# Kernel optimization log

Hardware: AMD Instinct MI355X
Metric: run time of the kernel (lower is better)

The kernel has to match this reference:

```python
import jax, jax.numpy as jnp
import numpy as np

B, T, I, E, K, J = 4, 4096, 1024, 16, 512, 1024


def setup_inputs() -> dict:
    key = jax.random.key(0)
    k1, k2, k3 = jax.random.split(key, 3)
    X = jax.random.normal(k1, (B, T, I), dtype=jnp.float32)
    ind = jax.random.randint(k2, (B, E, K), 0, T, dtype=jnp.int64)
    bound = 1.0 / np.sqrt(J)
    W = jax.random.uniform(k3, (E, I, J), dtype=jnp.float32, minval=-bound, maxval=bound)
    return {"X": X, "ind": ind, "W": W}


def reference(X, ind, W):
    Bs, Ts, Is = X.shape
    _, Es, Ks = ind.shape
    # gather tokens per expert: [B, E*K, I] -> [B, E, K, I]
    idx = ind.reshape(Bs, Es * Ks)
    Xg = jnp.take_along_axis(X, idx[:, :, None], axis=1).reshape(Bs, Es, Ks, Is)
    # per-expert GEMM
    Y = jnp.einsum('beki,eij->bekj', Xg, W)
    return Y
```

## Files before the change

kernel.cpp:

```cpp
#include <hip/hip_runtime.h>
#include <cstdint>
#include <cstddef>


typedef float    floatx4 __attribute__((ext_vector_type(4)));
typedef _Float16 half8   __attribute__((ext_vector_type(8)));

constexpr int Bc = 4, Tc = 4096, Ic = 1024, Ec = 16, Kc = 512, Jc = 1024;
constexpr int BM = 256, BN = 256, BK = 64, NT = 512;
constexpr int NKT = Ic / BK;
constexpr int UNIT = 16384;
constexpr int BOFF = 4 * UNIT;

__device__ __forceinline__ void async16(const void* g, void* l) {
  __builtin_amdgcn_global_load_lds(
      (const __attribute__((address_space(1))) uint32_t*)g,
      (__attribute__((address_space(3))) uint32_t*)l, 16, 0, 0);
}

__global__ void cvt_kernel(const float* __restrict__ X, _Float16* __restrict__ Xh, int n8,
                           const float* __restrict__ W, _Float16* __restrict__ WT) {
  __shared__ float tile[64][65];
  const int bidx = blockIdx.x;
  if (bidx >= Ec * 256) {
    int i = (bidx - Ec * 256) * blockDim.x + threadIdx.x;
    const int stride = 2048 * blockDim.x;
    for (; i < n8; i += stride) {
      floatx4 v0 = ((const floatx4*)X)[2 * i];
      floatx4 v1 = ((const floatx4*)X)[2 * i + 1];
      half8 h;
      h[0] = (_Float16)v0.x; h[1] = (_Float16)v0.y; h[2] = (_Float16)v0.z; h[3] = (_Float16)v0.w;
      h[4] = (_Float16)v1.x; h[5] = (_Float16)v1.y; h[6] = (_Float16)v1.z; h[7] = (_Float16)v1.w;
      ((half8*)Xh)[i] = h;
    }
    return;
  }
  const int bid = bidx;
  const int e  = bid >> 8;
  const int i0 = ((bid >> 4) & 15) * 64;
  const int j0 = (bid & 15) * 64;
  const int tid = threadIdx.x;
  const int r  = tid >> 4;
  const int c4 = tid & 15;
  const float* src = W + ((size_t)e << 20) + (size_t)i0 * Jc + j0;
#pragma unroll
  for (int s = 0; s < 4; s++) {
    int rr = r + s * 16;
    floatx4 v = *(const floatx4*)(src + (size_t)rr * Jc + c4 * 4);
    tile[rr][c4 * 4 + 0] = v.x; tile[rr][c4 * 4 + 1] = v.y;
    tile[rr][c4 * 4 + 2] = v.z; tile[rr][c4 * 4 + 3] = v.w;
  }
  __syncthreads();
  const int jj = tid >> 2;
  const int ig = tid & 3;
  half8 hv0, hv1;
#pragma unroll
  for (int q = 0; q < 8; q++) hv0[q] = (_Float16)tile[ig * 16 + q][jj];
#pragma unroll
  for (int q = 0; q < 8; q++) hv1[q] = (_Float16)tile[ig * 16 + 8 + q][jj];
  _Float16* dst = WT + ((size_t)e << 20) + (size_t)(j0 + jj) * Ic + i0 + ig * 16;
  ((half8*)dst)[0] = hv0;
  ((half8*)dst)[1] = hv1;
}

__global__ __launch_bounds__(NT, 2) void gemm_kernel(
    const int* __restrict__ ind32,
    const _Float16* __restrict__ Xh, const _Float16* __restrict__ WT,
    float* __restrict__ Y) {
  __shared__ alignas(16) unsigned char smem[8 * UNIT];
  __shared__ int rowid[BM];
  __shared__ int is64_s;
  float* lbuf = (float*)smem;
  char* smemc = (char*)smem;

  const int tid = threadIdx.x;
  const int bid = blockIdx.x;
  const int x = bid & 7, s = (bid >> 3) & 7, chunk = bid >> 6;
  const int g = chunk * 8 + x;
  const int e = g >> 2, nt = g & 3;
  const int b = s >> 1, mt = s & 1;
  const int be = b * Ec + e;
  const int k0 = mt * BM;
  const int j0 = nt * BN;

  if (tid < 64) {
    int v = ind32[2 * tid + 1];
    unsigned long long m = __ballot(v != 0);
    if (tid == 0) is64_s = (m == 0ULL) ? 1 : 0;
  }
  __syncthreads();
  if (tid < BM) {
    int idx = be * Kc + k0 + tid;
    rowid[tid] = is64_s ? ind32[2 * idx] : ind32[idx];
  }
  __syncthreads();

  const int lane = tid & 63;
  const int wave = tid >> 6;
  const int wmb = (wave >> 2) * 128;
  const int wnb = (wave & 3) * 64;
  const int quad = lane >> 4;
  const int tr = lane & 15;

  const _Float16* aSrc[2];
  const _Float16* bSrc[2];
#pragma unroll
  for (int q = 0; q < 2; q++) {
    const int sl = wave * 128 + q * 64 + lane;
    const int r2 = sl >> 3, p = sl & 7;
    const int pos = p ^ (r2 & 7);
    const int r = 2 * r2 + (pos >> 2);
    const int c = pos & 3;
    aSrc[q] = Xh + ((size_t)b * Tc + rowid[r]) * Ic + c * 8;
    bSrc[q] = WT + ((size_t)e * Jc + j0 + r) * Ic + c * 8;
  }
  const int wdst = wave * 2048;

  int offA[2][4], offB[4];
#pragma unroll
  for (int mh = 0; mh < 2; mh++)
#pragma unroll
    for (int mi = 0; mi < 4; mi++) {
      const int R = wmb + mh * 64 + mi * 16 + tr;
      const int r2 = R >> 1;
      offA[mh][mi] = r2 * 128 + ((((R & 1) << 2) | quad) ^ (r2 & 7)) * 16;
    }
#pragma unroll
  for (int ni = 0; ni < 4; ni++) {
    const int R = wnb + ni * 16 + tr;
    const int r2 = R >> 1;
    offB[ni] = r2 * 128 + ((((R & 1) << 2) | quad) ^ (r2 & 7)) * 16;
  }

  floatx4 acc[8][4];
#pragma unroll
  for (int mi = 0; mi < 8; mi++)
#pragma unroll
    for (int ni = 0; ni < 4; ni++) acc[mi][ni] = {0.f, 0.f, 0.f, 0.f};

#define STAGE_A(TT, KS) do { \
    char* d_ = smemc + ((2 * (TT) + (KS)) & 3) * UNIT + wdst; \
    async16(aSrc[0] + (TT) * 64 + (KS) * 32, d_); \
    async16(aSrc[1] + (TT) * 64 + (KS) * 32, d_ + 1024); \
  } while (0)
#define STAGE_B(TT, KS) do { \
    char* d_ = smemc + BOFF + ((2 * (TT) + (KS)) & 3) * UNIT + wdst; \
    async16(bSrc[0] + (TT) * 64 + (KS) * 32, d_); \
    async16(bSrc[1] + (TT) * 64 + (KS) * 32, d_ + 1024); \
  } while (0)

#define PHASE(SK, MH, STAGE_STMT, CLOSE_STMT) do { \
    const char* Ab_ = smemc + (SK) * UNIT; \
    const char* Bb_ = smemc + BOFF + (SK) * UNIT; \
    half8 af_[4], bf_[4]; \
    _Pragma("unroll") \
    for (int mi_ = 0; mi_ < 4; mi_++) af_[mi_] = *(const half8*)(Ab_ + offA[MH][mi_]); \
    _Pragma("unroll") \
    for (int ni_ = 0; ni_ < 4; ni_++) bf_[ni_] = *(const half8*)(Bb_ + offB[ni_]); \
    STAGE_STMT \
    __builtin_amdgcn_s_barrier(); \
    asm volatile("s_waitcnt lgkmcnt(0)" ::: "memory"); \
    __builtin_amdgcn_sched_barrier(0); \
    __builtin_amdgcn_s_setprio(1); \
    _Pragma("unroll") \
    for (int mi_ = 0; mi_ < 4; mi_++) \
      _Pragma("unroll") \
      for (int ni_ = 0; ni_ < 4; ni_++) \
        acc[(MH) * 4 + mi_][ni_] = __builtin_amdgcn_mfma_f32_16x16x32_f16( \
            af_[mi_], bf_[ni_], acc[(MH) * 4 + mi_][ni_], 0, 0, 0); \
    __builtin_amdgcn_s_setprio(0); \
    CLOSE_STMT \
    __builtin_amdgcn_s_barrier(); \
  } while (0)

  STAGE_A(0, 0); STAGE_B(0, 0);
  STAGE_A(0, 1); STAGE_B(0, 1);
  STAGE_A(1, 0); STAGE_B(1, 0);
  asm volatile("s_waitcnt vmcnt(4)" ::: "memory");
  __builtin_amdgcn_s_barrier();

#pragma unroll 2
  for (int t = 0; t < NKT; t++) {
    const int sk0 = (2 * t) & 3;
    const int sk1 = sk0 + 1;
    const bool f1 = (t + 1 < NKT);
    const bool f2 = (t + 2 < NKT);
    PHASE(sk0, 0, { if (f1) STAGE_A(t + 1, 1); }, {});
    PHASE(sk0, 1, { if (f1) STAGE_B(t + 1, 1); }, {});
    PHASE(sk1, 0, { if (f2) STAGE_A(t + 2, 0); }, {});
    PHASE(sk1, 1, { if (f2) STAGE_B(t + 2, 0); },
          { if (t == NKT - 2) { asm volatile("s_waitcnt vmcnt(0)" ::: "memory"); }
            else if (t < NKT - 2) { asm volatile("s_waitcnt vmcnt(4)" ::: "memory"); } });
  }
#undef PHASE
#undef STAGE_A
#undef STAGE_B

  constexpr int LST = 257;
  float* Yb = Y + (size_t)be * Kc * Jc;
#pragma unroll
  for (int pass = 0; pass < 8; pass++) {
    if ((wave >> 2) == (pass >> 2)) {
#pragma unroll
      for (int h = 0; h < 2; h++) {
        const int mi = (pass & 3) * 2 + h;
        const int rr = h * 16 + quad * 4;
#pragma unroll
        for (int ni = 0; ni < 4; ni++) {
          const int col = wnb + ni * 16 + tr;
#pragma unroll
          for (int r = 0; r < 4; r++)
            lbuf[(rr + r) * LST + col] = acc[mi][ni][r];
        }
      }
    }
    __syncthreads();
#pragma unroll
    for (int it = 0; it < 4; it++) {
      const int idx = tid + it * NT;
      const int rr = idx >> 6, c4 = idx & 63;
      floatx4 v = *(const floatx4*)&lbuf[rr * LST + c4 * 4];
      *(floatx4*)&Yb[(size_t)(k0 + pass * 32 + rr) * Jc + j0 + c4 * 4] = v;
    }
    __syncthreads();
  }
}

extern "C" void kernel_launch(void* const* d_in, const int* in_sizes, int n_in,
                              void* d_out, int out_size, void* d_ws, size_t ws_size,
                              hipStream_t stream) {
  const float* X = (const float*)d_in[0];
  const int* ind = (const int*)d_in[1];
  const float* W = (const float*)d_in[2];
  float* Y = (float*)d_out;

  const size_t nx = (size_t)Bc * Tc * Ic;
  _Float16* Xh = (_Float16*)d_ws;
  _Float16* WT = Xh + nx;

  cvt_kernel<<<Ec * 256 + 2048, 256, 0, stream>>>(X, Xh, (int)(nx / 8), W, WT);
  const int gemm_grid = (Bc * Ec) * (Kc / BM) * (Jc / BN);
  gemm_kernel<<<gemm_grid, NT, 0, stream>>>(ind, Xh, WT, Y);
}
```

Measured before the change: 314.4 us.

## Restructure GEMM main loop to share B fragments and cut barriers per k-tile

Replaces the four barrier-separated phases per k-tile with two half-steps. Each half-step loads the B fragments once and reuses them across both M halves, and stage issues are interleaved with the LDS fragment loads. The last two iterations are peeled so the steady-state loop has no prefetch conditionals. This cuts LDS traffic and the number of barriers per iteration, but drops the explicit lgkmcnt waits and sched_barrier. Instruction ordering is left to the compiler, and register pressure rises from holding three fragment arrays.

```diff
diff --git a/kernel.cpp b/kernel.cpp
--- a/kernel.cpp
+++ b/kernel.cpp
@@ -149,28 +149,25 @@
     async16(bSrc[1] + (TT) * 64 + (KS) * 32, d_ + 1024); \
   } while (0)
 
-#define PHASE(SK, MH, STAGE_STMT, CLOSE_STMT) do { \
+#define LDAF(DST, SK, MH) do { \
     const char* Ab_ = smemc + (SK) * UNIT; \
+    _Pragma("unroll") \
+    for (int mi_ = 0; mi_ < 4; mi_++) DST[mi_] = *(const half8*)(Ab_ + offA[MH][mi_]); \
+  } while (0)
+#define LDBF(DST, SK) do { \
     const char* Bb_ = smemc + BOFF + (SK) * UNIT; \
-    half8 af_[4], bf_[4]; \
     _Pragma("unroll") \
-    for (int mi_ = 0; mi_ < 4; mi_++) af_[mi_] = *(const half8*)(Ab_ + offA[MH][mi_]); \
-    _Pragma("unroll") \
-    for (int ni_ = 0; ni_ < 4; ni_++) bf_[ni_] = *(const half8*)(Bb_ + offB[ni_]); \
-    STAGE_STMT \
-    __builtin_amdgcn_s_barrier(); \
-    asm volatile("s_waitcnt lgkmcnt(0)" ::: "memory"); \
-    __builtin_amdgcn_sched_barrier(0); \
+    for (int ni_ = 0; ni_ < 4; ni_++) DST[ni_] = *(const half8*)(Bb_ + offB[ni_]); \
+  } while (0)
+#define MFMA16(MH, AF, BF) do { \
     __builtin_amdgcn_s_setprio(1); \
     _Pragma("unroll") \
     for (int mi_ = 0; mi_ < 4; mi_++) \
       _Pragma("unroll") \
       for (int ni_ = 0; ni_ < 4; ni_++) \
         acc[(MH) * 4 + mi_][ni_] = __builtin_amdgcn_mfma_f32_16x16x32_f16( \
-            af_[mi_], bf_[ni_], acc[(MH) * 4 + mi_][ni_], 0, 0, 0); \
+            AF[mi_], BF[ni_], acc[(MH) * 4 + mi_][ni_], 0, 0, 0); \
     __builtin_amdgcn_s_setprio(0); \
-    CLOSE_STMT \
-    __builtin_amdgcn_s_barrier(); \
   } while (0)
 
   STAGE_A(0, 0); STAGE_B(0, 0);
@@ -179,22 +176,68 @@
   asm volatile("s_waitcnt vmcnt(4)" ::: "memory");
   __builtin_amdgcn_s_barrier();
 
-#pragma unroll 2
-  for (int t = 0; t < NKT; t++) {
-    const int sk0 = (2 * t) & 3;
-    const int sk1 = sk0 + 1;
-    const bool f1 = (t + 1 < NKT);
-    const bool f2 = (t + 2 < NKT);
-    PHASE(sk0, 0, { if (f1) STAGE_A(t + 1, 1); }, {});
-    PHASE(sk0, 1, { if (f1) STAGE_B(t + 1, 1); }, {});
-    PHASE(sk1, 0, { if (f2) STAGE_A(t + 2, 0); }, {});
-    PHASE(sk1, 1, { if (f2) STAGE_B(t + 2, 0); },
-          { if (t == NKT - 2) { asm volatile("s_waitcnt vmcnt(0)" ::: "memory"); }
-            else if (t < NKT - 2) { asm volatile("s_waitcnt vmcnt(4)" ::: "memory"); } });
-  }
-#undef PHASE
+  for (int t = 0; t < NKT - 2; ++t) {
+    const int sk0 = (2 * t) & 3, sk1 = sk0 + 1;
+    half8 af0[4], af1[4], bf[4];
+    LDAF(af0, sk0, 0);
+    LDBF(bf, sk0);
+    STAGE_A(t + 1, 1);
+    LDAF(af1, sk0, 1);
+    STAGE_B(t + 1, 1);
+    MFMA16(0, af0, bf);
+    MFMA16(1, af1, bf);
+    __builtin_amdgcn_s_barrier();
+    LDAF(af1, sk1, 1);
+    LDBF(bf, sk1);
+    STAGE_A(t + 2, 0);
+    LDAF(af0, sk1, 0);
+    STAGE_B(t + 2, 0);
+    MFMA16(1, af1, bf);
+    MFMA16(0, af0, bf);
+    asm volatile("s_waitcnt vmcnt(4)" ::: "memory");
+    __builtin_amdgcn_s_barrier();
+  }
+  {
+    const int t = NKT - 2;
+    const int sk0 = (2 * t) & 3, sk1 = sk0 + 1;
+    half8 af0[4], af1[4], bf[4];
+    LDAF(af0, sk0, 0);
+    LDBF(bf, sk0);
+    STAGE_A(t + 1, 1);
+    LDAF(af1, sk0, 1);
+    STAGE_B(t + 1, 1);
+    MFMA16(0, af0, bf);
+    MFMA16(1, af1, bf);
+    __builtin_amdgcn_s_barrier();
+    LDAF(af1, sk1, 1);
+    LDBF(bf, sk1);
+    LDAF(af0, sk1, 0);
+    MFMA16(1, af1, bf);
+    MFMA16(0, af0, bf);
+    asm volatile("s_waitcnt vmcnt(0)" ::: "memory");
+    __builtin_amdgcn_s_barrier();
+  }
+  {
+    const int t = NKT - 1;
+    const int sk0 = (2 * t) & 3, sk1 = sk0 + 1;
+    half8 af0[4], af1[4], bf[4];
+    LDAF(af0, sk0, 0);
+    LDBF(bf, sk0);
+    LDAF(af1, sk0, 1);
+    MFMA16(0, af0, bf);
+    MFMA16(1, af1, bf);
+    LDAF(af1, sk1, 1);
+    LDBF(bf, sk1);
+    LDAF(af0, sk1, 0);
+    MFMA16(1, af1, bf);
+    MFMA16(0, af0, bf);
+  }
+  __syncthreads();
+#undef MFMA16
+#undef LDBF
+#undef LDAF
+#undef STAGE_B
 #undef STAGE_A
-#undef STAGE_B
 
   constexpr int LST = 257;
   float* Yb = Y + (size_t)be * Kc * Jc;
```

New measurement: 309.9 us. About the same (-1.4%).

## Shrink LDS ring to 80KB with 3-slot A, 2-slot B pipeline for higher occupancy

Applied to the files above, without the earlier changes.

Restructures the software pipeline so each phase consumes a full 32-wide k-step across all 8 M sub-tiles. A uses a 3-slot ring and B a 2-slot ring, with the loop unrolled by 6 to keep slot indices static. Shared memory drops from 128KB to 80KB and the row-id scratch is folded into the ring. Launch bounds are raised to 4 waves per SIMD so more blocks can be resident and memory latency is hidden better. The costs are more register pressure from holding 8 A fragments under the tighter register budget, and a shallower B prefetch distance.

```diff
diff --git a/kernel.cpp b/kernel.cpp
--- a/kernel.cpp
+++ b/kernel.cpp
@@ -7,10 +7,10 @@
 typedef _Float16 half8   __attribute__((ext_vector_type(8)));
 
 constexpr int Bc = 4, Tc = 4096, Ic = 1024, Ec = 16, Kc = 512, Jc = 1024;
-constexpr int BM = 256, BN = 256, BK = 64, NT = 512;
-constexpr int NKT = Ic / BK;
+constexpr int BM = 256, BN = 256, NT = 512;
 constexpr int UNIT = 16384;
-constexpr int BOFF = 4 * UNIT;
+constexpr int A_RING = 3 * UNIT;
+constexpr int SMEM_BYTES = A_RING + 2 * UNIT;
 
 __device__ __forceinline__ void async16(const void* g, void* l) {
   __builtin_amdgcn_global_load_lds(
@@ -63,15 +63,14 @@
   ((half8*)dst)[1] = hv1;
 }
 
-__global__ __launch_bounds__(NT, 2) void gemm_kernel(
+__global__ __launch_bounds__(NT, 4) void gemm_kernel(
     const int* __restrict__ ind32,
     const _Float16* __restrict__ Xh, const _Float16* __restrict__ WT,
     float* __restrict__ Y) {
-  __shared__ alignas(16) unsigned char smem[8 * UNIT];
-  __shared__ int rowid[BM];
-  __shared__ int is64_s;
+  __shared__ alignas(16) unsigned char smem[SMEM_BYTES];
+  char* smemc = (char*)smem;
+  int* itmp = (int*)smem;
   float* lbuf = (float*)smem;
-  char* smemc = (char*)smem;
 
   const int tid = threadIdx.x;
   const int bid = blockIdx.x;
@@ -86,12 +85,13 @@
   if (tid < 64) {
     int v = ind32[2 * tid + 1];
     unsigned long long m = __ballot(v != 0);
-    if (tid == 0) is64_s = (m == 0ULL) ? 1 : 0;
-  }
-  __syncthreads();
+    if (tid == 0) itmp[256] = (m == 0ULL) ? 1 : 0;
+  }
+  __syncthreads();
+  const int is64 = itmp[256];
   if (tid < BM) {
     int idx = be * Kc + k0 + tid;
-    rowid[tid] = is64_s ? ind32[2 * idx] : ind32[idx];
+    itmp[tid] = is64 ? ind32[2 * idx] : ind32[idx];
   }
   __syncthreads();
 
@@ -111,20 +111,19 @@
     const int pos = p ^ (r2 & 7);
     const int r = 2 * r2 + (pos >> 2);
     const int c = pos & 3;
-    aSrc[q] = Xh + ((size_t)b * Tc + rowid[r]) * Ic + c * 8;
+    aSrc[q] = Xh + ((size_t)b * Tc + itmp[r]) * Ic + c * 8;
     bSrc[q] = WT + ((size_t)e * Jc + j0 + r) * Ic + c * 8;
   }
   const int wdst = wave * 2048;
-
-  int offA[2][4], offB[4];
-#pragma unroll
-  for (int mh = 0; mh < 2; mh++)
-#pragma unroll
-    for (int mi = 0; mi < 4; mi++) {
-      const int R = wmb + mh * 64 + mi * 16 + tr;
-      const int r2 = R >> 1;
-      offA[mh][mi] = r2 * 128 + ((((R & 1) << 2) | quad) ^ (r2 & 7)) * 16;
-    }
+  __syncthreads();
+
+  int offA[8], offB[4];
+#pragma unroll
+  for (int mi = 0; mi < 8; mi++) {
+    const int R = wmb + mi * 16 + tr;
+    const int r2 = R >> 1;
+    offA[mi] = r2 * 128 + ((((R & 1) << 2) | quad) ^ (r2 & 7)) * 16;
+  }
 #pragma unroll
   for (int ni = 0; ni < 4; ni++) {
     const int R = wnb + ni * 16 + tr;
@@ -138,63 +137,62 @@
 #pragma unroll
     for (int ni = 0; ni < 4; ni++) acc[mi][ni] = {0.f, 0.f, 0.f, 0.f};
 
-#define STAGE_A(TT, KS) do { \
-    char* d_ = smemc + ((2 * (TT) + (KS)) & 3) * UNIT + wdst; \
-    async16(aSrc[0] + (TT) * 64 + (KS) * 32, d_); \
-    async16(aSrc[1] + (TT) * 64 + (KS) * 32, d_ + 1024); \
+#define STAGE_A(U, SL) do { \
+    char* d_ = smemc + (SL) * UNIT + wdst; \
+    async16(aSrc[0] + (U) * 32, d_); \
+    async16(aSrc[1] + (U) * 32, d_ + 1024); \
   } while (0)
-#define STAGE_B(TT, KS) do { \
-    char* d_ = smemc + BOFF + ((2 * (TT) + (KS)) & 3) * UNIT + wdst; \
-    async16(bSrc[0] + (TT) * 64 + (KS) * 32, d_); \
-    async16(bSrc[1] + (TT) * 64 + (KS) * 32, d_ + 1024); \
+#define STAGE_B(U, SL) do { \
+    char* d_ = smemc + A_RING + (SL) * UNIT + wdst; \
+    async16(bSrc[0] + (U) * 32, d_); \
+    async16(bSrc[1] + (U) * 32, d_ + 1024); \
   } while (0)
 
-#define PHASE(SK, MH, STAGE_STMT, CLOSE_STMT) do { \
-    const char* Ab_ = smemc + (SK) * UNIT; \
-    const char* Bb_ = smemc + BOFF + (SK) * UNIT; \
-    half8 af_[4], bf_[4]; \
+#define PHASE(ASL, BSL, DOB, DOA, CLOSE) do { \
+    const char* Ab_ = smemc + (ASL) * UNIT; \
+    const char* Bb_ = smemc + A_RING + (BSL) * UNIT; \
+    half8 af_[8], bf_[4]; \
     _Pragma("unroll") \
-    for (int mi_ = 0; mi_ < 4; mi_++) af_[mi_] = *(const half8*)(Ab_ + offA[MH][mi_]); \
+    for (int mi_ = 0; mi_ < 8; mi_++) af_[mi_] = *(const half8*)(Ab_ + offA[mi_]); \
     _Pragma("unroll") \
     for (int ni_ = 0; ni_ < 4; ni_++) bf_[ni_] = *(const half8*)(Bb_ + offB[ni_]); \
-    STAGE_STMT \
+    DOB; DOA; \
     __builtin_amdgcn_s_barrier(); \
     asm volatile("s_waitcnt lgkmcnt(0)" ::: "memory"); \
     __builtin_amdgcn_sched_barrier(0); \
     __builtin_amdgcn_s_setprio(1); \
     _Pragma("unroll") \
-    for (int mi_ = 0; mi_ < 4; mi_++) \
+    for (int mi_ = 0; mi_ < 8; mi_++) \
       _Pragma("unroll") \
       for (int ni_ = 0; ni_ < 4; ni_++) \
-        acc[(MH) * 4 + mi_][ni_] = __builtin_amdgcn_mfma_f32_16x16x32_f16( \
-            af_[mi_], bf_[ni_], acc[(MH) * 4 + mi_][ni_], 0, 0, 0); \
+        acc[mi_][ni_] = __builtin_amdgcn_mfma_f32_16x16x32_f16( \
+            af_[mi_], bf_[ni_], acc[mi_][ni_], 0, 0, 0); \
     __builtin_amdgcn_s_setprio(0); \
-    CLOSE_STMT \
+    CLOSE; \
     __builtin_amdgcn_s_barrier(); \
   } while (0)
 
-  STAGE_A(0, 0); STAGE_B(0, 0);
-  STAGE_A(0, 1); STAGE_B(0, 1);
-  STAGE_A(1, 0); STAGE_B(1, 0);
-  asm volatile("s_waitcnt vmcnt(4)" ::: "memory");
+  STAGE_A(0, 0); STAGE_B(0, 0); STAGE_A(1, 1);
+  asm volatile("s_waitcnt vmcnt(2)" ::: "memory");
   __builtin_amdgcn_s_barrier();
 
-#pragma unroll 2
-  for (int t = 0; t < NKT; t++) {
-    const int sk0 = (2 * t) & 3;
-    const int sk1 = sk0 + 1;
-    const bool f1 = (t + 1 < NKT);
-    const bool f2 = (t + 2 < NKT);
-    PHASE(sk0, 0, { if (f1) STAGE_A(t + 1, 1); }, {});
-    PHASE(sk0, 1, { if (f1) STAGE_B(t + 1, 1); }, {});
-    PHASE(sk1, 0, { if (f2) STAGE_A(t + 2, 0); }, {});
-    PHASE(sk1, 1, { if (f2) STAGE_B(t + 2, 0); },
-          { if (t == NKT - 2) { asm volatile("s_waitcnt vmcnt(0)" ::: "memory"); }
-            else if (t < NKT - 2) { asm volatile("s_waitcnt vmcnt(4)" ::: "memory"); } });
-  }
+  for (int u0 = 0; u0 < 30; u0 += 6) {
+#pragma unroll
+    for (int i = 0; i < 6; i++) {
+      const int u = u0 + i;
+      PHASE(i % 3, i & 1,
+            STAGE_B(u + 1, (i + 1) & 1),
+            STAGE_A(u + 2, (i + 2) % 3),
+            asm volatile("s_waitcnt vmcnt(2)" ::: "memory"));
+    }
+  }
+  PHASE(0, 0, STAGE_B(31, 1), (void)0,
+        asm volatile("s_waitcnt vmcnt(0)" ::: "memory"));
+  PHASE(1, 1, (void)0, (void)0, (void)0);
+  __syncthreads();
 #undef PHASE
+#undef STAGE_B
 #undef STAGE_A
-#undef STAGE_B
 
   constexpr int LST = 257;
   float* Yb = Y + (size_t)be * Kc * Jc;
```

Result: slower. 1.058 ms (+236.4%).
